# Kernel optimization log

Measured on AMD Instinct MI355X. Metric: run time of the kernel, lower is better.

The kernel has to match this reference:

```python
import jax, jax.numpy as jnp
import numpy as np

H = 1024      # hidden_size
NH = 16       # n_heads
DK = 64       # d_kv


def setup_inputs() -> dict:
    key = jax.random.key(0)
    k1, k2, k3, k4, k5 = jax.random.split(key, 5)
    x = jax.random.normal(k1, (4, 2048, H), dtype=jnp.float32)
    # dense1: hidden -> 3*n_heads*d_kv
    W1 = jax.random.normal(k2, (H, 3 * NH * DK), dtype=jnp.float32) / np.sqrt(H)
    b1 = jax.random.normal(k3, (3 * NH * DK,), dtype=jnp.float32) * 0.02
    # dense2: n_heads*d_kv -> hidden
    W2 = jax.random.normal(k4, (NH * DK, H), dtype=jnp.float32) / np.sqrt(NH * DK)
    b2 = jax.random.normal(k5, (H,), dtype=jnp.float32) * 0.02
    return {"x": x, "W1": W1, "b1": b1, "W2": W2, "b2": b2}


def reference(x, W1, b1, W2, b2):
    B, S, _ = x.shape
    scale = 1.0 / np.sqrt(DK)
    qkv = x @ W1 + b1                                   # [B,S,3*NH*DK]
    qkv = qkv.reshape(B, S, 3, NH, DK)
    q, k, v = jnp.moveaxis(qkv, 2, 0)                   # each [B,S,NH,DK]
    q = q.transpose(0, 2, 1, 3)                         # [B,NH,S,DK]
    k = k.transpose(0, 2, 1, 3)
    v = v.transpose(0, 2, 1, 3)
    scores = jnp.einsum('bhqd,bhkd->bhqk', q, k) * scale  # [B,NH,S,S]
    attn = jax.nn.softmax(scores, axis=-1)
    ctx = jnp.einsum('bhqk,bhkd->bhqd', attn, v)        # [B,NH,S,DK]
    ctx = ctx.transpose(0, 2, 1, 3).reshape(B, S, NH * DK)
    return ctx @ W2 + b2
```

## Files before the change

kernel.cpp:

```cpp
#include <hip/hip_runtime.h>
#include <hip/hip_bf16.h>


typedef __hip_bfloat16 bf16;
typedef __attribute__((ext_vector_type(8))) short bf16x8;
typedef __attribute__((ext_vector_type(4))) float f32x4;

#define B_   4
#define S_   2048
#define H_   1024
#define NH_  16
#define DK_  64
#define M_   8192
#define N1_  3072
#define K_   1024

#define SCALE_Q 0.18033688f

typedef const __attribute__((address_space(1))) void* gas_t;
typedef __attribute__((address_space(3))) void* las_t;
#define G2L16(g, l) __builtin_amdgcn_global_load_lds((gas_t)(g), (las_t)(l), 16, 0, 0)

__device__ __forceinline__ float b2f(bf16 v) { return __bfloat162float(v); }

__global__ __launch_bounds__(256) void conv_x(const float* __restrict__ X,
                                              bf16* __restrict__ Xb)
{
    size_t i = ((size_t)blockIdx.x * 256 + threadIdx.x) * 8;
    float4 lo = *(const float4*)&X[i];
    float4 hi = *(const float4*)&X[i + 4];
    bf16 t[8] __attribute__((aligned(16)));
    t[0] = __float2bfloat16(lo.x); t[1] = __float2bfloat16(lo.y);
    t[2] = __float2bfloat16(lo.z); t[3] = __float2bfloat16(lo.w);
    t[4] = __float2bfloat16(hi.x); t[5] = __float2bfloat16(hi.y);
    t[6] = __float2bfloat16(hi.z); t[7] = __float2bfloat16(hi.w);
    *(bf16x8*)&Xb[i] = *(const bf16x8*)t;
}

__global__ __launch_bounds__(256) void conv_wT(const float* __restrict__ W,
                                               bf16* __restrict__ WT,
                                               int Kdim, int Ndim)
{
    __shared__ bf16 T[64][72];
    const int tid = threadIdx.x;
    const int n0 = blockIdx.x * 64, k0 = blockIdx.y * 64;
    const int kr = tid >> 4, nc = (tid & 15) * 4;
    #pragma unroll
    for (int p = 0; p < 4; ++p) {
        float4 v = *(const float4*)&W[(size_t)(k0 + kr + p * 16) * Ndim + n0 + nc];
        T[nc + 0][kr + p * 16] = __float2bfloat16(v.x);
        T[nc + 1][kr + p * 16] = __float2bfloat16(v.y);
        T[nc + 2][kr + p * 16] = __float2bfloat16(v.z);
        T[nc + 3][kr + p * 16] = __float2bfloat16(v.w);
    }
    __syncthreads();
    const int nr = tid >> 2, kc = (tid & 3) * 16;
    *(bf16x8*)&WT[(size_t)(n0 + nr) * Kdim + k0 + kc]     = *(const bf16x8*)&T[nr][kc];
    *(bf16x8*)&WT[(size_t)(n0 + nr) * Kdim + k0 + kc + 8] = *(const bf16x8*)&T[nr][kc + 8];
}

__device__ __forceinline__ void qkv_epilogue(
    const f32x4 acc[4][4], const float* __restrict__ B1,
    bf16* __restrict__ Qp, bf16* __restrict__ Kp, bf16* __restrict__ Vt,
    int n0, int m0, int wm, int wn, int quad, int col)
{
    const int which = n0 >> 10;
    const int bb = m0 >> 11;
    if (which == 2) {
        #pragma unroll
        for (int i = 0; i < 4; ++i) {
            int s = (m0 & (S_ - 1)) + wm * 64 + i * 16 + quad * 4;
            #pragma unroll
            for (int j = 0; j < 4; ++j) {
                int n = n0 + wn * 64 + j * 16 + col;
                int h = (n >> 6) & 15, d = n & 63;
                float bv = B1[n];
                bf16 t[4] __attribute__((aligned(8)));
                #pragma unroll
                for (int r = 0; r < 4; ++r) t[r] = __float2bfloat16(acc[i][j][r] + bv);
                *(uint2*)&Vt[(((size_t)(bb * NH_ + h)) * DK_ + d) * S_ + s] = *(const uint2*)t;
            }
        }
    } else {
        bf16* dst = which ? Kp : Qp;
        const float sc = which ? 1.0f : SCALE_Q;
        #pragma unroll
        for (int i = 0; i < 4; ++i) {
            #pragma unroll
            for (int r = 0; r < 4; ++r) {
                int s = (m0 & (S_ - 1)) + wm * 64 + i * 16 + quad * 4 + r;
                #pragma unroll
                for (int j = 0; j < 4; ++j) {
                    int n = n0 + wn * 64 + j * 16 + col;
                    int h = (n >> 6) & 15, d = n & 63;
                    dst[(((size_t)(bb * NH_ + h)) * S_ + s) * DK_ + d] =
                        __float2bfloat16((acc[i][j][r] + B1[n]) * sc);
                }
            }
        }
    }
}

__global__ __launch_bounds__(256) void gemm_qkv_mfma2(
    const bf16* __restrict__ Xb, const bf16* __restrict__ W1T,
    const float* __restrict__ B1,
    bf16* __restrict__ Qp, bf16* __restrict__ Kp, bf16* __restrict__ Vt)
{
    __shared__ bf16 As[128 * 32];
    __shared__ bf16 Bs[128 * 32];

    const int tid = threadIdx.x;
    const int lane = tid & 63, wv = tid >> 6;
    const int col = lane & 15, quad = lane >> 4;
    const int wm = wv >> 1, wn = wv & 1;
    const int n0 = blockIdx.x * 128, m0 = blockIdx.y * 128;

    f32x4 acc[4][4] = {};

    const bf16* Ag = Xb  + (size_t)m0 * K_;
    const bf16* Bg = W1T + (size_t)n0 * K_;

    for (int k0 = 0; k0 < K_; k0 += 32) {
        #pragma unroll
        for (int h = 0; h < 2; ++h) {
            int idx = tid + h * 256;
            int row = idx >> 2, c = (idx & 3) * 8;
            G2L16(Ag + (size_t)row * K_ + k0 + c, As + (size_t)idx * 8);
            G2L16(Bg + (size_t)row * K_ + k0 + c, Bs + (size_t)idx * 8);
        }
        __syncthreads();

        bf16x8 af[4], bfr[4];
        #pragma unroll
        for (int i = 0; i < 4; ++i)
            af[i] = *(const bf16x8*)&As[(wm * 64 + i * 16 + col) * 32 + quad * 8];
        #pragma unroll
        for (int j = 0; j < 4; ++j)
            bfr[j] = *(const bf16x8*)&Bs[(wn * 64 + j * 16 + col) * 32 + quad * 8];

        #pragma unroll
        for (int i = 0; i < 4; ++i)
            #pragma unroll
            for (int j = 0; j < 4; ++j)
                acc[i][j] = __builtin_amdgcn_mfma_f32_16x16x32_bf16(af[i], bfr[j], acc[i][j], 0, 0, 0);
        __syncthreads();
    }
    qkv_epilogue(acc, B1, Qp, Kp, Vt, n0, m0, wm, wn, quad, col);
}

__global__ __launch_bounds__(256) void gemm_qkv_mfma(
    const float* __restrict__ X, const bf16* __restrict__ W1T,
    const float* __restrict__ B1,
    bf16* __restrict__ Qp, bf16* __restrict__ Kp, bf16* __restrict__ Vt)
{
    __shared__ bf16 As[128 * 32];
    __shared__ bf16 Bs[128 * 32];

    const int tid = threadIdx.x;
    const int lane = tid & 63, wv = tid >> 6;
    const int col = lane & 15, quad = lane >> 4;
    const int wm = wv >> 1, wn = wv & 1;
    const int n0 = blockIdx.x * 128, m0 = blockIdx.y * 128;

    f32x4 acc[4][4] = {};

    const float* Ag = X   + (size_t)m0 * K_;
    const bf16*  Bg = W1T + (size_t)n0 * K_;

    for (int k0 = 0; k0 < K_; k0 += 32) {
        #pragma unroll
        for (int h = 0; h < 2; ++h) {
            int idx = tid + h * 256;
            int row = idx >> 2, c = (idx & 3) * 8;
            G2L16(Bg + (size_t)row * K_ + k0 + c, Bs + (size_t)idx * 8);
        }
        #pragma unroll
        for (int h = 0; h < 2; ++h) {
            int idx = tid + h * 256;
            int row = idx >> 2, c = (idx & 3) * 8;
            float4 lo = *(const float4*)&Ag[(size_t)row * K_ + k0 + c];
            float4 hi = *(const float4*)&Ag[(size_t)row * K_ + k0 + c + 4];
            bf16 t[8] __attribute__((aligned(16)));
            t[0] = __float2bfloat16(lo.x); t[1] = __float2bfloat16(lo.y);
            t[2] = __float2bfloat16(lo.z); t[3] = __float2bfloat16(lo.w);
            t[4] = __float2bfloat16(hi.x); t[5] = __float2bfloat16(hi.y);
            t[6] = __float2bfloat16(hi.z); t[7] = __float2bfloat16(hi.w);
            *(bf16x8*)&As[(size_t)idx * 8] = *(const bf16x8*)t;
        }
        __syncthreads();

        bf16x8 af[4], bfr[4];
        #pragma unroll
        for (int i = 0; i < 4; ++i)
            af[i] = *(const bf16x8*)&As[(wm * 64 + i * 16 + col) * 32 + quad * 8];
        #pragma unroll
        for (int j = 0; j < 4; ++j)
            bfr[j] = *(const bf16x8*)&Bs[(wn * 64 + j * 16 + col) * 32 + quad * 8];

        #pragma unroll
        for (int i = 0; i < 4; ++i)
            #pragma unroll
            for (int j = 0; j < 4; ++j)
                acc[i][j] = __builtin_amdgcn_mfma_f32_16x16x32_bf16(af[i], bfr[j], acc[i][j], 0, 0, 0);
        __syncthreads();
    }
    qkv_epilogue(acc, B1, Qp, Kp, Vt, n0, m0, wm, wn, quad, col);
}

__global__ __launch_bounds__(256) void attn_mfma(
    const bf16* __restrict__ Q, const bf16* __restrict__ K,
    const bf16* __restrict__ Vt, bf16* __restrict__ CTX)
{
    __shared__ bf16 Ks[64][72];
    __shared__ bf16 Vs[64][72];
    __shared__ bf16 Ps[4][16][72];

    const int tid  = threadIdx.x;
    const int wv   = tid >> 6;
    const int lane = tid & 63;
    const int col  = lane & 15;
    const int quad = lane >> 4;

    const int bh = blockIdx.y;
    const int q0 = blockIdx.x * 64;

    const bf16* Qg  = Q  + (size_t)bh * S_ * DK_;
    const bf16* Kg  = K  + (size_t)bh * S_ * DK_;
    const bf16* Vtg = Vt + (size_t)bh * DK_ * S_;

    const short oneb = (short)0x3F80;
    const bf16x8 ones = {oneb, oneb, oneb, oneb, oneb, oneb, oneb, oneb};

    const int qrow = q0 + wv * 16 + col;
    bf16x8 qf[2];
    qf[0] = *(const bf16x8*)&Qg[(size_t)qrow * DK_ + quad * 8];
    qf[1] = *(const bf16x8*)&Qg[(size_t)qrow * DK_ + 32 + quad * 8];

    f32x4 o[4] = {};
    f32x4 l_acc = {0.f, 0.f, 0.f, 0.f};

    const int sr = tid >> 3;
    const int e0 = (tid & 7) * 8;

    bf16x8 kreg[2], vreg[2];
    #pragma unroll
    for (int half = 0; half < 2; ++half) {
        int r = sr + half * 32;
        kreg[half] = *(const bf16x8*)&Kg[(size_t)r * DK_ + e0];
        vreg[half] = *(const bf16x8*)&Vtg[(size_t)r * S_ + e0];
    }

    for (int kt = 0; kt < S_ / 64; ++kt) {
        #pragma unroll
        for (int half = 0; half < 2; ++half) {
            int r = sr + half * 32;
            *(bf16x8*)&Ks[r][e0] = kreg[half];
            *(bf16x8*)&Vs[r][e0] = vreg[half];
        }
        __syncthreads();

        if (kt + 1 < S_ / 64) {
            #pragma unroll
            for (int half = 0; half < 2; ++half) {
                int r = sr + half * 32;
                kreg[half] = *(const bf16x8*)&Kg[(size_t)((kt + 1) * 64 + r) * DK_ + e0];
                vreg[half] = *(const bf16x8*)&Vtg[(size_t)r * S_ + (kt + 1) * 64 + e0];
            }
        }

        f32x4 s[4];
        #pragma unroll
        for (int nsub = 0; nsub < 4; ++nsub) {
            const bf16* kb = &Ks[nsub * 16 + col][0];
            f32x4 a = {0.f, 0.f, 0.f, 0.f};
            a = __builtin_amdgcn_mfma_f32_16x16x32_bf16(qf[0], *(const bf16x8*)&kb[quad * 8], a, 0, 0, 0);
            a = __builtin_amdgcn_mfma_f32_16x16x32_bf16(qf[1], *(const bf16x8*)&kb[32 + quad * 8], a, 0, 0, 0);
            s[nsub] = a;
        }

        #pragma unroll
        for (int nsub = 0; nsub < 4; ++nsub)
            #pragma unroll
            for (int reg = 0; reg < 4; ++reg)
                Ps[wv][quad * 4 + reg][nsub * 16 + col] =
                    __float2bfloat16(exp2f(s[nsub][reg]));

        bf16x8 pf[2];
        pf[0] = *(const bf16x8*)&Ps[wv][col][quad * 8];
        pf[1] = *(const bf16x8*)&Ps[wv][col][32 + quad * 8];

        l_acc = __builtin_amdgcn_mfma_f32_16x16x32_bf16(pf[0], ones, l_acc, 0, 0, 0);
        l_acc = __builtin_amdgcn_mfma_f32_16x16x32_bf16(pf[1], ones, l_acc, 0, 0, 0);

        #pragma unroll
        for (int dsub = 0; dsub < 4; ++dsub) {
            const bf16* vb = &Vs[dsub * 16 + col][0];
            o[dsub] = __builtin_amdgcn_mfma_f32_16x16x32_bf16(pf[0], *(const bf16x8*)&vb[quad * 8], o[dsub], 0, 0, 0);
            o[dsub] = __builtin_amdgcn_mfma_f32_16x16x32_bf16(pf[1], *(const bf16x8*)&vb[32 + quad * 8], o[dsub], 0, 0, 0);
        }
        __syncthreads();
    }

    const int b = bh >> 4, h = bh & 15;
    #pragma unroll
    for (int reg = 0; reg < 4; ++reg) {
        float inv = 1.f / l_acc[reg];
        int srow = q0 + wv * 16 + quad * 4 + reg;
        #pragma unroll
        for (int dsub = 0; dsub < 4; ++dsub) {
            CTX[((size_t)(b * S_ + srow)) * H_ + h * DK_ + dsub * 16 + col] =
                __float2bfloat16(o[dsub][reg] * inv);
        }
    }
}

__global__ __launch_bounds__(256) void gemm_out_mfma(
    const bf16* __restrict__ Cx, const bf16* __restrict__ W2T,
    const float* __restrict__ B2, float* __restrict__ OUT)
{
    __shared__ bf16 As[128 * 32];
    __shared__ bf16 Bs[128 * 32];

    const int tid = threadIdx.x;
    const int lane = tid & 63, wv = tid >> 6;
    const int col = lane & 15, quad = lane >> 4;
    const int wm = wv >> 1, wn = wv & 1;
    const int n0 = blockIdx.x * 128, m0 = blockIdx.y * 128;

    f32x4 acc[4][4] = {};

    const bf16* Ag = Cx  + (size_t)m0 * K_;
    const bf16* Bg = W2T + (size_t)n0 * K_;

    for (int k0 = 0; k0 < K_; k0 += 32) {
        #pragma unroll
        for (int h = 0; h < 2; ++h) {
            int idx = tid + h * 256;
            int row = idx >> 2, c = (idx & 3) * 8;
            G2L16(Ag + (size_t)row * K_ + k0 + c, As + (size_t)idx * 8);
            G2L16(Bg + (size_t)row * K_ + k0 + c, Bs + (size_t)idx * 8);
        }
        __syncthreads();

        bf16x8 af[4], bfr[4];
        #pragma unroll
        for (int i = 0; i < 4; ++i)
            af[i] = *(const bf16x8*)&As[(wm * 64 + i * 16 + col) * 32 + quad * 8];
        #pragma unroll
        for (int j = 0; j < 4; ++j)
            bfr[j] = *(const bf16x8*)&Bs[(wn * 64 + j * 16 + col) * 32 + quad * 8];

        #pragma unroll
        for (int i = 0; i < 4; ++i)
            #pragma unroll
            for (int j = 0; j < 4; ++j)
                acc[i][j] = __builtin_amdgcn_mfma_f32_16x16x32_bf16(af[i], bfr[j], acc[i][j], 0, 0, 0);
        __syncthreads();
    }

    #pragma unroll
    for (int i = 0; i < 4; ++i) {
        #pragma unroll
        for (int r = 0; r < 4; ++r) {
            int m = m0 + wm * 64 + i * 16 + quad * 4 + r;
            #pragma unroll
            for (int j = 0; j < 4; ++j) {
                int n = n0 + wn * 64 + j * 16 + col;
                OUT[(size_t)m * H_ + n] = acc[i][j][r] + B2[n];
            }
        }
    }
}

extern "C" void kernel_launch(void* const* d_in, const int* in_sizes, int n_in,
                              void* d_out, int out_size, void* d_ws, size_t ws_size,
                              hipStream_t stream)
{
    const float* X  = (const float*)d_in[0];
    const float* W1 = (const float*)d_in[1];
    const float* B1 = (const float*)d_in[2];
    const float* W2 = (const float*)d_in[3];
    const float* B2 = (const float*)d_in[4];
    float* OUT = (float*)d_out;

    const size_t QE = (size_t)B_ * NH_ * S_ * DK_;
    bf16* Qw  = (bf16*)d_ws;
    bf16* Kw  = Qw + QE;
    bf16* Vw  = Kw + QE;
    bf16* Rw  = Vw + QE;
    bf16* W1T = Rw;
    bf16* Cw  = Rw;
    bf16* W2T = Qw;
    bf16* Xb  = Rw + QE;

    const bool fast = ws_size >= 5 * QE * sizeof(bf16);

    conv_wT<<<dim3(N1_ / 64, K_ / 64), 256, 0, stream>>>(W1, W1T, K_, N1_);
    if (fast) {
        conv_x<<<dim3((int)(QE / (256 * 8))), 256, 0, stream>>>(X, Xb);
        gemm_qkv_mfma2<<<dim3(N1_ / 128, M_ / 128), 256, 0, stream>>>(Xb, W1T, B1, Qw, Kw, Vw);
    } else {
        gemm_qkv_mfma<<<dim3(N1_ / 128, M_ / 128), 256, 0, stream>>>(X, W1T, B1, Qw, Kw, Vw);
    }
    attn_mfma<<<dim3(S_ / 64, B_ * NH_), 256, 0, stream>>>(Qw, Kw, Vw, Cw);
    conv_wT<<<dim3(H_ / 64, K_ / 64), 256, 0, stream>>>(W2, W2T, K_, H_);
    gemm_out_mfma<<<dim3(H_ / 128, M_ / 128), 256, 0, stream>>>(Cw, W2T, B2, OUT);
}
```

Measured before the change: 338.1 us.

## Double attention query tile to 128 rows with 512 threads and transposed MFMA

The attention kernel now uses 8 waves per block, covering 128 query rows. Each K/V tile staged in shared memory is reused by twice as many queries, and each thread does a single 16-byte load per tile. The score and PV MFMAs swap operands so that each lane holds a query row's results. This lets exp values be written to shared memory as packed 8-byte stores and lets context rows be stored as packed uint2. A manual round-to-nearest-even bf16 pack helper replaces per-element conversions in the conversion, QKV epilogue and attention code, at the cost of halving the block count and possibly hitting register limits under launch_bounds(512,8).

```diff
diff --git a/kernel.cpp b/kernel.cpp
--- a/kernel.cpp
+++ b/kernel.cpp
@@ -23,18 +23,24 @@
 
 __device__ __forceinline__ float b2f(bf16 v) { return __bfloat162float(v); }
 
+__device__ __forceinline__ unsigned pk2(float a, float b) {
+    unsigned ua = __float_as_uint(a);
+    unsigned ub = __float_as_uint(b);
+    ua += 0x7FFFu + ((ua >> 16) & 1u);
+    ub += 0x7FFFu + ((ub >> 16) & 1u);
+    return (ua >> 16) | (ub & 0xFFFF0000u);
+}
+
 __global__ __launch_bounds__(256) void conv_x(const float* __restrict__ X,
                                               bf16* __restrict__ Xb)
 {
     size_t i = ((size_t)blockIdx.x * 256 + threadIdx.x) * 8;
     float4 lo = *(const float4*)&X[i];
     float4 hi = *(const float4*)&X[i + 4];
-    bf16 t[8] __attribute__((aligned(16)));
-    t[0] = __float2bfloat16(lo.x); t[1] = __float2bfloat16(lo.y);
-    t[2] = __float2bfloat16(lo.z); t[3] = __float2bfloat16(lo.w);
-    t[4] = __float2bfloat16(hi.x); t[5] = __float2bfloat16(hi.y);
-    t[6] = __float2bfloat16(hi.z); t[7] = __float2bfloat16(hi.w);
-    *(bf16x8*)&Xb[i] = *(const bf16x8*)t;
+    uint4 u;
+    u.x = pk2(lo.x, lo.y); u.y = pk2(lo.z, lo.w);
+    u.z = pk2(hi.x, hi.y); u.w = pk2(hi.z, hi.w);
+    *(uint4*)&Xb[i] = u;
 }
 
 __global__ __launch_bounds__(256) void conv_wT(const float* __restrict__ W,
@@ -75,10 +81,10 @@
                 int n = n0 + wn * 64 + j * 16 + col;
                 int h = (n >> 6) & 15, d = n & 63;
                 float bv = B1[n];
-                bf16 t[4] __attribute__((aligned(8)));
-                #pragma unroll
-                for (int r = 0; r < 4; ++r) t[r] = __float2bfloat16(acc[i][j][r] + bv);
-                *(uint2*)&Vt[(((size_t)(bb * NH_ + h)) * DK_ + d) * S_ + s] = *(const uint2*)t;
+                uint2 t;
+                t.x = pk2(acc[i][j][0] + bv, acc[i][j][1] + bv);
+                t.y = pk2(acc[i][j][2] + bv, acc[i][j][3] + bv);
+                *(uint2*)&Vt[(((size_t)(bb * NH_ + h)) * DK_ + d) * S_ + s] = t;
             }
         }
     } else {
@@ -180,12 +186,10 @@
             int row = idx >> 2, c = (idx & 3) * 8;
             float4 lo = *(const float4*)&Ag[(size_t)row * K_ + k0 + c];
             float4 hi = *(const float4*)&Ag[(size_t)row * K_ + k0 + c + 4];
-            bf16 t[8] __attribute__((aligned(16)));
-            t[0] = __float2bfloat16(lo.x); t[1] = __float2bfloat16(lo.y);
-            t[2] = __float2bfloat16(lo.z); t[3] = __float2bfloat16(lo.w);
-            t[4] = __float2bfloat16(hi.x); t[5] = __float2bfloat16(hi.y);
-            t[6] = __float2bfloat16(hi.z); t[7] = __float2bfloat16(hi.w);
-            *(bf16x8*)&As[(size_t)idx * 8] = *(const bf16x8*)t;
+            uint4 u;
+            u.x = pk2(lo.x, lo.y); u.y = pk2(lo.z, lo.w);
+            u.z = pk2(hi.x, hi.y); u.w = pk2(hi.z, hi.w);
+            *(uint4*)&As[(size_t)idx * 8] = u;
         }
         __syncthreads();
 
@@ -207,13 +211,13 @@
     qkv_epilogue(acc, B1, Qp, Kp, Vt, n0, m0, wm, wn, quad, col);
 }
 
-__global__ __launch_bounds__(256) void attn_mfma(
+__global__ __launch_bounds__(512, 8) void attn_mfma(
     const bf16* __restrict__ Q, const bf16* __restrict__ K,
     const bf16* __restrict__ Vt, bf16* __restrict__ CTX)
 {
     __shared__ bf16 Ks[64][72];
     __shared__ bf16 Vs[64][72];
-    __shared__ bf16 Ps[4][16][72];
+    __shared__ bf16 Ps[8][16][72];
 
     const int tid  = threadIdx.x;
     const int wv   = tid >> 6;
@@ -222,7 +226,7 @@
     const int quad = lane >> 4;
 
     const int bh = blockIdx.y;
-    const int q0 = blockIdx.x * 64;
+    const int q0 = blockIdx.x * 128;
 
     const bf16* Qg  = Q  + (size_t)bh * S_ * DK_;
     const bf16* Kg  = K  + (size_t)bh * S_ * DK_;
@@ -242,75 +246,56 @@
     const int sr = tid >> 3;
     const int e0 = (tid & 7) * 8;
 
-    bf16x8 kreg[2], vreg[2];
+    bf16x8 kreg = *(const bf16x8*)&Kg[(size_t)sr * DK_ + e0];
+    bf16x8 vreg = *(const bf16x8*)&Vtg[(size_t)sr * S_ + e0];
+
+    for (int kt = 0; kt < S_ / 64; ++kt) {
+        *(bf16x8*)&Ks[sr][e0] = kreg;
+        *(bf16x8*)&Vs[sr][e0] = vreg;
+        __syncthreads();
+
+        if (kt + 1 < S_ / 64) {
+            kreg = *(const bf16x8*)&Kg[(size_t)((kt + 1) * 64 + sr) * DK_ + e0];
+            vreg = *(const bf16x8*)&Vtg[(size_t)sr * S_ + (kt + 1) * 64 + e0];
+        }
+
+        #pragma unroll
+        for (int cs = 0; cs < 4; ++cs) {
+            const bf16* kb = &Ks[cs * 16 + col][0];
+            f32x4 a = {0.f, 0.f, 0.f, 0.f};
+            a = __builtin_amdgcn_mfma_f32_16x16x32_bf16(*(const bf16x8*)&kb[quad * 8],      qf[0], a, 0, 0, 0);
+            a = __builtin_amdgcn_mfma_f32_16x16x32_bf16(*(const bf16x8*)&kb[32 + quad * 8], qf[1], a, 0, 0, 0);
+            uint2 p;
+            p.x = pk2(exp2f(a[0]), exp2f(a[1]));
+            p.y = pk2(exp2f(a[2]), exp2f(a[3]));
+            *(uint2*)&Ps[wv][col][cs * 16 + quad * 4] = p;
+        }
+
+        bf16x8 pf0 = *(const bf16x8*)&Ps[wv][col][quad * 8];
+        bf16x8 pf1 = *(const bf16x8*)&Ps[wv][col][32 + quad * 8];
+
+        l_acc = __builtin_amdgcn_mfma_f32_16x16x32_bf16(ones, pf0, l_acc, 0, 0, 0);
+        l_acc = __builtin_amdgcn_mfma_f32_16x16x32_bf16(ones, pf1, l_acc, 0, 0, 0);
+
+        #pragma unroll
+        for (int ds = 0; ds < 4; ++ds) {
+            const bf16* vb = &Vs[ds * 16 + col][0];
+            o[ds] = __builtin_amdgcn_mfma_f32_16x16x32_bf16(*(const bf16x8*)&vb[quad * 8],      pf0, o[ds], 0, 0, 0);
+            o[ds] = __builtin_amdgcn_mfma_f32_16x16x32_bf16(*(const bf16x8*)&vb[32 + quad * 8], pf1, o[ds], 0, 0, 0);
+        }
+        __syncthreads();
+    }
+
+    const int b = bh >> 4, h = bh & 15;
+    const float inv = 1.f / l_acc[0];
+    const int srow = q0 + wv * 16 + col;
+    bf16* crow = CTX + ((size_t)(b * S_ + srow)) * H_ + h * DK_;
     #pragma unroll
-    for (int half = 0; half < 2; ++half) {
-        int r = sr + half * 32;
-        kreg[half] = *(const bf16x8*)&Kg[(size_t)r * DK_ + e0];
-        vreg[half] = *(const bf16x8*)&Vtg[(size_t)r * S_ + e0];
-    }
-
-    for (int kt = 0; kt < S_ / 64; ++kt) {
-        #pragma unroll
-        for (int half = 0; half < 2; ++half) {
-            int r = sr + half * 32;
-            *(bf16x8*)&Ks[r][e0] = kreg[half];
-            *(bf16x8*)&Vs[r][e0] = vreg[half];
-        }
-        __syncthreads();
-
-        if (kt + 1 < S_ / 64) {
-            #pragma unroll
-            for (int half = 0; half < 2; ++half) {
-                int r = sr + half * 32;
-                kreg[half] = *(const bf16x8*)&Kg[(size_t)((kt + 1) * 64 + r) * DK_ + e0];
-                vreg[half] = *(const bf16x8*)&Vtg[(size_t)r * S_ + (kt + 1) * 64 + e0];
-            }
-        }
-
-        f32x4 s[4];
-        #pragma unroll
-        for (int nsub = 0; nsub < 4; ++nsub) {
-            const bf16* kb = &Ks[nsub * 16 + col][0];
-            f32x4 a = {0.f, 0.f, 0.f, 0.f};
-            a = __builtin_amdgcn_mfma_f32_16x16x32_bf16(qf[0], *(const bf16x8*)&kb[quad * 8], a, 0, 0, 0);
-            a = __builtin_amdgcn_mfma_f32_16x16x32_bf16(qf[1], *(const bf16x8*)&kb[32 + quad * 8], a, 0, 0, 0);
-            s[nsub] = a;
-        }
-
-        #pragma unroll
-        for (int nsub = 0; nsub < 4; ++nsub)
-            #pragma unroll
-            for (int reg = 0; reg < 4; ++reg)
-                Ps[wv][quad * 4 + reg][nsub * 16 + col] =
-                    __float2bfloat16(exp2f(s[nsub][reg]));
-
-        bf16x8 pf[2];
-        pf[0] = *(const bf16x8*)&Ps[wv][col][quad * 8];
-        pf[1] = *(const bf16x8*)&Ps[wv][col][32 + quad * 8];
-
-        l_acc = __builtin_amdgcn_mfma_f32_16x16x32_bf16(pf[0], ones, l_acc, 0, 0, 0);
-        l_acc = __builtin_amdgcn_mfma_f32_16x16x32_bf16(pf[1], ones, l_acc, 0, 0, 0);
-
-        #pragma unroll
-        for (int dsub = 0; dsub < 4; ++dsub) {
-            const bf16* vb = &Vs[dsub * 16 + col][0];
-            o[dsub] = __builtin_amdgcn_mfma_f32_16x16x32_bf16(pf[0], *(const bf16x8*)&vb[quad * 8], o[dsub], 0, 0, 0);
-            o[dsub] = __builtin_amdgcn_mfma_f32_16x16x32_bf16(pf[1], *(const bf16x8*)&vb[32 + quad * 8], o[dsub], 0, 0, 0);
-        }
-        __syncthreads();
-    }
-
-    const int b = bh >> 4, h = bh & 15;
-    #pragma unroll
-    for (int reg = 0; reg < 4; ++reg) {
-        float inv = 1.f / l_acc[reg];
-        int srow = q0 + wv * 16 + quad * 4 + reg;
-        #pragma unroll
-        for (int dsub = 0; dsub < 4; ++dsub) {
-            CTX[((size_t)(b * S_ + srow)) * H_ + h * DK_ + dsub * 16 + col] =
-                __float2bfloat16(o[dsub][reg] * inv);
-        }
+    for (int ds = 0; ds < 4; ++ds) {
+        uint2 t;
+        t.x = pk2(o[ds][0] * inv, o[ds][1] * inv);
+        t.y = pk2(o[ds][2] * inv, o[ds][3] * inv);
+        *(uint2*)&crow[ds * 16 + quad * 4] = t;
     }
 }
 
@@ -402,7 +387,7 @@
     } else {
         gemm_qkv_mfma<<<dim3(N1_ / 128, M_ / 128), 256, 0, stream>>>(X, W1T, B1, Qw, Kw, Vw);
     }
-    attn_mfma<<<dim3(S_ / 64, B_ * NH_), 256, 0, stream>>>(Qw, Kw, Vw, Cw);
+    attn_mfma<<<dim3(S_ / 128, B_ * NH_), 512, 0, stream>>>(Qw, Kw, Vw, Cw);
     conv_wT<<<dim3(H_ / 64, K_ / 64), 256, 0, stream>>>(W2, W2T, K_, H_);
     gemm_out_mfma<<<dim3(H_ / 128, M_ / 128), 256, 0, stream>>>(Cw, W2T, B2, OUT);
 }
```

After: 318.0 us. -6.0%, faster.
